# Kernel optimization log

Hardware: AMD Instinct MI355X
Metric: run time of the kernel (lower is better)

The kernel has to match this reference:

```python
import jax, jax.numpy as jnp
import numpy as np

B = 4096          # batch of vectors
D = 768           # embedding_size
P = 96            # partition (number of sub-quantizers)
C = 256           # centroids per partition
SD = D // P       # sub-vector dim = 8


def setup_inputs() -> dict:
    key = jax.random.key(0)
    k1, k2 = jax.random.split(key)
    vecs = jax.random.normal(k1, (B, D), dtype=jnp.float32)
    # nn.Parameter(torch.empty(P, C, SD).uniform_(-0.1, 0.1))
    codebook = jax.random.uniform(k2, (P, C, SD), dtype=jnp.float32,
                                  minval=-0.1, maxval=0.1)
    return {"vecs": vecs, "codebook": codebook}


def _quantize(vecs, codebook):
    # vecs: [B, D] -> [B, P, SD]
    v = vecs.reshape(vecs.shape[0], P, SD)
    # proba = -sum((v - c)^2) expanded to avoid the [B,P,C,SD] intermediate:
    # ||v||^2 - 2 v.c + ||c||^2  per (b, p, c)
    v_sq = jnp.sum(v * v, axis=-1, keepdims=True)            # [B, P, 1]
    c_sq = jnp.sum(codebook * codebook, axis=-1)             # [P, C]
    vc = jnp.einsum('bpd,pcd->bpc', v, codebook)             # [B, P, C]
    proba = -(v_sq - 2.0 * vc + c_sq[None])                  # [B, P, C]
    assign = jax.nn.softmax(proba, axis=-1)                  # [B, P, C]
    # straight-through estimator: hard one-hot fwd, soft grad
    index = jnp.argmax(assign, axis=-1)                      # [B, P]
    assign_hard = jax.nn.one_hot(index, C, dtype=assign.dtype)
    assign_ste = jax.lax.stop_gradient(assign_hard - assign) + assign
    # reconstruction: [B,P,C] @ [P,C,SD] -> [B,P,SD] -> [B,D]
    q = jnp.einsum('bpc,pcd->bpd', assign_ste, codebook)
    return q.reshape(vecs.shape[0], -1)


def reference(vecs, codebook):
    return _quantize(vecs, codebook)
```

## Files before the change

### kernel.cpp

```cpp
#include <hip/hip_runtime.h>
#include <cmath>

constexpr int B  = 4096;
constexpr int D  = 768;
constexpr int P  = 96;
constexpr int C  = 256;
constexpr int SD = 8;

constexpr int TPB  = 256;
constexpr int WPB  = 4;
constexpr int CPW  = C / WPB;
constexpr int ROWS = 4;

__device__ __forceinline__ float tree8(float q0, float q1, float q2, float q3,
                                       float q4, float q5, float q6, float q7)
{
#pragma clang fp contract(off)
    return ((q0 + q1) + (q2 + q3)) + ((q4 + q5) + (q6 + q7));
}

__device__ __forceinline__ float proba_np(const float* __restrict__ cbf,
                                          const float* __restrict__ csq,
                                          int c, float4 va, float4 vb, float vsq)
{
#pragma clang fp contract(off)
    float4 ca = ((const float4*)cbf)[2 * c];
    float4 cb = ((const float4*)cbf)[2 * c + 1];
    float p0 = va.x * ca.x, p1 = va.y * ca.y, p2 = va.z * ca.z, p3 = va.w * ca.w;
    float p4 = vb.x * cb.x, p5 = vb.y * cb.y, p6 = vb.z * cb.z, p7 = vb.w * cb.w;
    float l0 = p0 + p4, l1 = p1 + p5, l2 = p2 + p6, l3 = p3 + p7;
    float vc = (l0 + l2) + (l1 + l3);
    float tt = vsq - 2.0f * vc;
    float u  = tt + csq[c];
    return -u;
}

__device__ __forceinline__
int exact_search(const float* __restrict__ cbf, const float* __restrict__ csq,
                 float4 va, float4 vb, float vsq)
{
#pragma clang fp contract(off)
    float best = -3.402823466e38f, second = -3.402823466e38f;
    int bi = 0;
    for (int c = 0; c < C; ++c) {
        float pr = proba_np(cbf, csq, c, va, vb, vsq);
        if (pr > best)        { second = best; best = pr; bi = c; }
        else if (pr > second) { second = pr; }
    }
    int idx = bi;

    if (best - second <= 1.0e-6f) {
        float m = best;
        float r0[8] = {0,0,0,0,0,0,0,0};
        float r1[8] = {0,0,0,0,0,0,0,0};
        for (int cg = 0; cg < 16; ++cg) {
            #pragma unroll
            for (int j = 0; j < 8; ++j) {
                float pr = proba_np(cbf, csq, cg * 8 + j, va, vb, vsq);
                r0[j] += expf(pr - m);
            }
        }
        for (int cg = 16; cg < 32; ++cg) {
            #pragma unroll
            for (int j = 0; j < 8; ++j) {
                float pr = proba_np(cbf, csq, cg * 8 + j, va, vb, vsq);
                r1[j] += expf(pr - m);
            }
        }
        float sum = tree8(r0[0],r0[1],r0[2],r0[3],r0[4],r0[5],r0[6],r0[7])
                  + tree8(r1[0],r1[1],r1[2],r1[3],r1[4],r1[5],r1[6],r1[7]);
        float abest = -1.0f;
        int   ai    = 0;
        for (int c = 0; c < C; ++c) {
            float pr = proba_np(cbf, csq, c, va, vb, vsq);
            float e  = expf(pr - m);
            float a  = e / sum;
            if (a > abest) { abest = a; ai = c; }
        }
        idx = ai;
    }
    return idx;
}

__global__ __launch_bounds__(TPB, 4)
void pq_split_kernel(const float* __restrict__ vecs,
                     const float* __restrict__ codebook,
                     float* __restrict__ out)
{
    __shared__ float  cbf [C * SD];
    __shared__ float  csqn[C];
    __shared__ float  csqh[C];
    __shared__ float2 part_bs[WPB][ROWS][64];
    __shared__ int    part_i [WPB][ROWS][64];

    const int p = blockIdx.x;
    const int t = threadIdx.x;
    const int w = t >> 6;
    const int l = t & 63;
    const int rowbase = blockIdx.y * (64 * ROWS);

    const float* cg = codebook + ((size_t)p * C + t) * SD;
    float4 cra = ((const float4*)cg)[0];
    float4 crb = ((const float4*)cg)[1];

    float4 va[ROWS], vb[ROWS];
    #pragma unroll
    for (int r = 0; r < ROWS; ++r) {
        const float* vptr = vecs + (size_t)(rowbase + 64 * r + l) * D + (size_t)p * SD;
        va[r] = ((const float4*)vptr)[0];
        vb[r] = ((const float4*)vptr)[1];
    }

    {
#pragma clang fp contract(off)
        float q0 = cra.x*cra.x, q1 = cra.y*cra.y, q2 = cra.z*cra.z, q3 = cra.w*cra.w;
        float q4 = crb.x*crb.x, q5 = crb.y*crb.y, q6 = crb.z*crb.z, q7 = crb.w*crb.w;
        float s = tree8(q0,q1,q2,q3,q4,q5,q6,q7);
        csqn[t] = s;
        csqh[t] = -0.5f * s;
    }
    ((float4*)cbf)[2 * t]     = cra;
    ((float4*)cbf)[2 * t + 1] = crb;
    __syncthreads();

    float best[ROWS], second[ROWS];
    int   bi[ROWS];
    #pragma unroll
    for (int r = 0; r < ROWS; ++r) {
        best[r] = -3.402823466e38f; second[r] = -3.402823466e38f; bi[r] = 0;
    }

    const int c0 = w * CPW;
    #pragma unroll 4
    for (int ci = 0; ci < CPW; ++ci) {
        const int c = c0 + ci;
        float4 ca = ((const float4*)cbf)[2 * c];
        float4 cb = ((const float4*)cbf)[2 * c + 1];
        float  ch = csqh[c];
        #pragma unroll
        for (int r = 0; r < ROWS; ++r) {
            float s = fmaf(va[r].x, ca.x, ch);
            s = fmaf(va[r].y, ca.y, s);
            s = fmaf(va[r].z, ca.z, s);
            s = fmaf(va[r].w, ca.w, s);
            s = fmaf(vb[r].x, cb.x, s);
            s = fmaf(vb[r].y, cb.y, s);
            s = fmaf(vb[r].z, cb.z, s);
            s = fmaf(vb[r].w, cb.w, s);
            bool gt = s > best[r];
            second[r] = fmaxf(second[r], fminf(s, best[r]));
            bi[r]     = gt ? c : bi[r];
            best[r]   = fmaxf(s, best[r]);
        }
    }

    #pragma unroll
    for (int r = 0; r < ROWS; ++r) {
        part_bs[w][r][l] = make_float2(best[r], second[r]);
        part_i [w][r][l] = bi[r];
    }
    __syncthreads();

    {
        float Bst = -3.402823466e38f, Snd = -3.402823466e38f;
        int   I   = 0;
        #pragma unroll
        for (int ww = 0; ww < WPB; ++ww) {
            float2 bs = part_bs[ww][w][l];
            int    iw = part_i [ww][w][l];
            bool gt = bs.x > Bst;
            Snd = fmaxf(Snd, fminf(bs.x, Bst));
            Snd = fmaxf(Snd, bs.y);
            I   = gt ? iw : I;
            Bst = fmaxf(Bst, bs.x);
        }

        const int row = rowbase + t;
        int idx = I;
        if (Bst - Snd <= 2.0e-5f) {
            const float* vptr = vecs + (size_t)row * D + (size_t)p * SD;
            float4 xa = ((const float4*)vptr)[0];
            float4 xb = ((const float4*)vptr)[1];
            float q0 = xa.x*xa.x, q1 = xa.y*xa.y, q2 = xa.z*xa.z, q3 = xa.w*xa.w;
            float q4 = xb.x*xb.x, q5 = xb.y*xb.y, q6 = xb.z*xb.z, q7 = xb.w*xb.w;
            float vsq = tree8(q0,q1,q2,q3,q4,q5,q6,q7);
            idx = exact_search(cbf, csqn, xa, xb, vsq);
        }

        float4 o0 = ((const float4*)cbf)[2 * idx];
        float4 o1 = ((const float4*)cbf)[2 * idx + 1];
        float4* op = (float4*)(out + (size_t)row * D + (size_t)p * SD);
        op[0] = o0;
        op[1] = o1;
    }
}

extern "C" void kernel_launch(void* const* d_in, const int* in_sizes, int n_in,
                              void* d_out, int out_size, void* d_ws, size_t ws_size,
                              hipStream_t stream)
{
    const float* vecs     = (const float*)d_in[0];
    const float* codebook = (const float*)d_in[1];
    float*       out      = (float*)d_out;

    dim3 grid(P, B / (64 * ROWS));
    dim3 block(TPB);
    pq_split_kernel<<<grid, block, 0, stream>>>(vecs, codebook, out);
}
```

Before: 176.9 us.

## Scan codebook from registers via readlane, drop cross-wave reduction

Each wave now loads the full 256-entry codebook into registers, four segments of 64 lanes, and broadcasts centroid values with readlane. Every thread scans all centroids for two rows, rather than splitting centroids across four waves and merging partial results through shared memory. This removes LDS reads from the hot loop as well as the partial-result shared arrays and the merge step. In exchange each wave does four times more centroid work per row, rows per block go from 256 to 512 so there are half as many blocks, and the scalar readlane broadcasts may add latency.

Measured after the change: 212.7 us. 20.2% more time.

```diff
diff --git a/kernel.cpp b/kernel.cpp
--- a/kernel.cpp
+++ b/kernel.cpp
@@ -8,9 +8,9 @@
 constexpr int SD = 8;
 
 constexpr int TPB  = 256;
-constexpr int WPB  = 4;
-constexpr int CPW  = C / WPB;
-constexpr int ROWS = 4;
+constexpr int ROWS = 2;
+constexpr int SEGS = 4;
+constexpr int RPB  = TPB * ROWS;
 
 __device__ __forceinline__ float tree8(float q0, float q1, float q2, float q3,
                                        float q4, float q5, float q6, float q7)
@@ -82,46 +82,63 @@
     return idx;
 }
 
+__device__ __forceinline__ float rdlane(float x, int i)
+{
+    return __int_as_float(__builtin_amdgcn_readlane(__float_as_int(x), i));
+}
+
 __global__ __launch_bounds__(TPB, 4)
-void pq_split_kernel(const float* __restrict__ vecs,
-                     const float* __restrict__ codebook,
-                     float* __restrict__ out)
-{
-    __shared__ float  cbf [C * SD];
-    __shared__ float  csqn[C];
-    __shared__ float  csqh[C];
-    __shared__ float2 part_bs[WPB][ROWS][64];
-    __shared__ int    part_i [WPB][ROWS][64];
+void pq_regscan_kernel(const float* __restrict__ vecs,
+                       const float* __restrict__ codebook,
+                       float* __restrict__ out)
+{
+    __shared__ float cbf [C * SD];
+    __shared__ float csqn[C];
 
     const int p = blockIdx.x;
     const int t = threadIdx.x;
     const int w = t >> 6;
     const int l = t & 63;
-    const int rowbase = blockIdx.y * (64 * ROWS);
-
-    const float* cg = codebook + ((size_t)p * C + t) * SD;
-    float4 cra = ((const float4*)cg)[0];
-    float4 crb = ((const float4*)cg)[1];
+    const int rowbase = blockIdx.y * RPB;
+
+    float4 cA[SEGS], cB[SEGS];
+    #pragma unroll
+    for (int s = 0; s < SEGS; ++s) {
+        const float* cg = codebook + ((size_t)p * C + s * 64 + l) * SD;
+        cA[s] = ((const float4*)cg)[0];
+        cB[s] = ((const float4*)cg)[1];
+    }
 
     float4 va[ROWS], vb[ROWS];
     #pragma unroll
     for (int r = 0; r < ROWS; ++r) {
-        const float* vptr = vecs + (size_t)(rowbase + 64 * r + l) * D + (size_t)p * SD;
+        const float* vptr = vecs + (size_t)(rowbase + r * TPB + t) * D + (size_t)p * SD;
         va[r] = ((const float4*)vptr)[0];
         vb[r] = ((const float4*)vptr)[1];
     }
 
+    float ch[SEGS], q[SEGS];
+    #pragma unroll
+    for (int s = 0; s < SEGS; ++s) {
+#pragma clang fp contract(off)
+        float q0 = cA[s].x*cA[s].x, q1 = cA[s].y*cA[s].y;
+        float q2 = cA[s].z*cA[s].z, q3 = cA[s].w*cA[s].w;
+        float q4 = cB[s].x*cB[s].x, q5 = cB[s].y*cB[s].y;
+        float q6 = cB[s].z*cB[s].z, q7 = cB[s].w*cB[s].w;
+        q[s]  = tree8(q0,q1,q2,q3,q4,q5,q6,q7);
+        ch[s] = -0.5f * q[s];
+    }
+
     {
-#pragma clang fp contract(off)
-        float q0 = cra.x*cra.x, q1 = cra.y*cra.y, q2 = cra.z*cra.z, q3 = cra.w*cra.w;
-        float q4 = crb.x*crb.x, q5 = crb.y*crb.y, q6 = crb.z*crb.z, q7 = crb.w*crb.w;
-        float s = tree8(q0,q1,q2,q3,q4,q5,q6,q7);
-        csqn[t] = s;
-        csqh[t] = -0.5f * s;
-    }
-    ((float4*)cbf)[2 * t]     = cra;
-    ((float4*)cbf)[2 * t + 1] = crb;
-    __syncthreads();
+        float4 sa = cA[0], sb = cB[0];
+        float  sq = q[0];
+        if (w == 1) { sa = cA[1]; sb = cB[1]; sq = q[1]; }
+        if (w == 2) { sa = cA[2]; sb = cB[2]; sq = q[2]; }
+        if (w == 3) { sa = cA[3]; sb = cB[3]; sq = q[3]; }
+        ((float4*)cbf)[2 * t]     = sa;
+        ((float4*)cbf)[2 * t + 1] = sb;
+        csqn[t] = sq;
+    }
 
     float best[ROWS], second[ROWS];
     int   bi[ROWS];
@@ -130,63 +147,52 @@
         best[r] = -3.402823466e38f; second[r] = -3.402823466e38f; bi[r] = 0;
     }
 
-    const int c0 = w * CPW;
-    #pragma unroll 4
-    for (int ci = 0; ci < CPW; ++ci) {
-        const int c = c0 + ci;
-        float4 ca = ((const float4*)cbf)[2 * c];
-        float4 cb = ((const float4*)cbf)[2 * c + 1];
-        float  ch = csqh[c];
-        #pragma unroll
-        for (int r = 0; r < ROWS; ++r) {
-            float s = fmaf(va[r].x, ca.x, ch);
-            s = fmaf(va[r].y, ca.y, s);
-            s = fmaf(va[r].z, ca.z, s);
-            s = fmaf(va[r].w, ca.w, s);
-            s = fmaf(vb[r].x, cb.x, s);
-            s = fmaf(vb[r].y, cb.y, s);
-            s = fmaf(vb[r].z, cb.z, s);
-            s = fmaf(vb[r].w, cb.w, s);
-            bool gt = s > best[r];
-            second[r] = fmaxf(second[r], fminf(s, best[r]));
-            bi[r]     = gt ? c : bi[r];
-            best[r]   = fmaxf(s, best[r]);
-        }
-    }
+    #pragma unroll
+    for (int s = 0; s < SEGS; ++s) {
+        const float4 A  = cA[s];
+        const float4 Bb = cB[s];
+        const float  H  = ch[s];
+        #pragma unroll 4
+        for (int ci = 0; ci < 64; ++ci) {
+            const int c = s * 64 + ci;
+            float cax = rdlane(A.x,  ci), cay = rdlane(A.y,  ci);
+            float caz = rdlane(A.z,  ci), caw = rdlane(A.w,  ci);
+            float cbx = rdlane(Bb.x, ci), cby = rdlane(Bb.y, ci);
+            float cbz = rdlane(Bb.z, ci), cbw = rdlane(Bb.w, ci);
+            float chc = rdlane(H,    ci);
+            #pragma unroll
+            for (int r = 0; r < ROWS; ++r) {
+                float sv = fmaf(va[r].x, cax, chc);
+                sv = fmaf(va[r].y, cay, sv);
+                sv = fmaf(va[r].z, caz, sv);
+                sv = fmaf(va[r].w, caw, sv);
+                sv = fmaf(vb[r].x, cbx, sv);
+                sv = fmaf(vb[r].y, cby, sv);
+                sv = fmaf(vb[r].z, cbz, sv);
+                sv = fmaf(vb[r].w, cbw, sv);
+                bool gt = sv > best[r];
+                second[r] = fmaxf(second[r], fminf(sv, best[r]));
+                bi[r]     = gt ? c : bi[r];
+                best[r]   = fmaxf(sv, best[r]);
+            }
+        }
+    }
+
+    __syncthreads();
 
     #pragma unroll
     for (int r = 0; r < ROWS; ++r) {
-        part_bs[w][r][l] = make_float2(best[r], second[r]);
-        part_i [w][r][l] = bi[r];
-    }
-    __syncthreads();
-
-    {
-        float Bst = -3.402823466e38f, Snd = -3.402823466e38f;
-        int   I   = 0;
-        #pragma unroll
-        for (int ww = 0; ww < WPB; ++ww) {
-            float2 bs = part_bs[ww][w][l];
-            int    iw = part_i [ww][w][l];
-            bool gt = bs.x > Bst;
-            Snd = fmaxf(Snd, fminf(bs.x, Bst));
-            Snd = fmaxf(Snd, bs.y);
-            I   = gt ? iw : I;
-            Bst = fmaxf(Bst, bs.x);
-        }
-
-        const int row = rowbase + t;
-        int idx = I;
-        if (Bst - Snd <= 2.0e-5f) {
-            const float* vptr = vecs + (size_t)row * D + (size_t)p * SD;
-            float4 xa = ((const float4*)vptr)[0];
-            float4 xb = ((const float4*)vptr)[1];
-            float q0 = xa.x*xa.x, q1 = xa.y*xa.y, q2 = xa.z*xa.z, q3 = xa.w*xa.w;
-            float q4 = xb.x*xb.x, q5 = xb.y*xb.y, q6 = xb.z*xb.z, q7 = xb.w*xb.w;
+        const int row = rowbase + r * TPB + t;
+        int idx = bi[r];
+        if (best[r] - second[r] <= 2.0e-5f) {
+#pragma clang fp contract(off)
+            float q0 = va[r].x*va[r].x, q1 = va[r].y*va[r].y;
+            float q2 = va[r].z*va[r].z, q3 = va[r].w*va[r].w;
+            float q4 = vb[r].x*vb[r].x, q5 = vb[r].y*vb[r].y;
+            float q6 = vb[r].z*vb[r].z, q7 = vb[r].w*vb[r].w;
             float vsq = tree8(q0,q1,q2,q3,q4,q5,q6,q7);
-            idx = exact_search(cbf, csqn, xa, xb, vsq);
-        }
-
+            idx = exact_search(cbf, csqn, va[r], vb[r], vsq);
+        }
         float4 o0 = ((const float4*)cbf)[2 * idx];
         float4 o1 = ((const float4*)cbf)[2 * idx + 1];
         float4* op = (float4*)(out + (size_t)row * D + (size_t)p * SD);
@@ -203,7 +209,7 @@
     const float* codebook = (const float*)d_in[1];
     float*       out      = (float*)d_out;
 
-    dim3 grid(P, B / (64 * ROWS));
+    dim3 grid(P, B / RPB);
     dim3 block(TPB);
-    pq_split_kernel<<<grid, block, 0, stream>>>(vecs, codebook, out);
-}
+    pq_regscan_kernel<<<grid, block, 0, stream>>>(vecs, codebook, out);
+}
```
